# Optimization experiments

Measured on AMD Instinct MI355X. Metric: run time of the kernel, lower is better.

## Reference

```python
import jax, jax.numpy as jnp
import numpy as np

NUM_HEADS = 16

def setup_inputs() -> dict:
    key = jax.random.key(0)
    k1, k2, k3 = jax.random.split(key, 3)
    D = 1024
    return {
        "hidden_states": jax.random.normal(k1, (2, 2048, D), dtype=jnp.float32),
        "c_attn_w": jax.random.normal(k2, (D, 3 * D), dtype=jnp.float32) * 0.02,
        "c_attn_b": jnp.zeros((3 * D,), dtype=jnp.float32),
        "c_proj_w": jax.random.normal(k3, (D, D), dtype=jnp.float32) * 0.02,
        "c_proj_b": jnp.zeros((D,), dtype=jnp.float32),
    }

def reference(hidden_states, c_attn_w, c_attn_b, c_proj_w, c_proj_b):
    B, S, D = hidden_states.shape
    H = NUM_HEADS
    hd = D // H
    # Conv1D: x @ W + b, then split into q, k, v
    qkv = hidden_states @ c_attn_w + c_attn_b  # [B, S, 3D]
    q, k, v = jnp.split(qkv, 3, axis=-1)
    q = q.reshape(B, S, H, hd).transpose(0, 2, 1, 3)  # [B, H, S, hd]
    k = k.reshape(B, S, H, hd).transpose(0, 2, 1, 3)
    v = v.reshape(B, S, H, hd).transpose(0, 2, 1, 3)
    # scaled QK^T
    scores = jnp.einsum("bhqd,bhkd->bhqk", q, k) / jnp.asarray(hd ** 0.5, q.dtype)
    # causal mask (tril), masked positions set to dtype min per original code
    causal = jnp.tril(jnp.ones((S, S), dtype=bool))
    mask_value = jnp.finfo(scores.dtype).min
    scores = jnp.where(causal[None, None], scores, mask_value)
    attn = jax.nn.softmax(scores, axis=-1)
    out = jnp.einsum("bhqk,bhkd->bhqd", attn, v)  # [B, H, S, hd]
    out = out.transpose(0, 2, 1, 3).reshape(B, S, D)
    out = out @ c_proj_w + c_proj_b
    return out
```

## Files before the change

### kernel.cpp

```cpp
#include <hip/hip_runtime.h>
#include <hip/hip_bf16.h>
#include <math.h>

#define B_ 2
#define S_ 2048
#define D_ 1024
#define H_ 16
#define HD 64
#define M_ (B_ * S_)
#define N_QKV (3 * D_)

typedef short short8 __attribute__((ext_vector_type(8)));
typedef float floatx4 __attribute__((ext_vector_type(4)));

static __device__ __forceinline__ unsigned short f2bf(float x) {
    __hip_bfloat16 h = __float2bfloat16(x);
    unsigned short u;
    __builtin_memcpy(&u, &h, sizeof(u));
    return u;
}
static __device__ __forceinline__ float bf2f(unsigned short b) {
    union { unsigned u; float f; } v; v.u = ((unsigned)b) << 16;
    return v.f;
}
static __device__ __forceinline__ void split2(float x, unsigned short& h, unsigned short& l) {
    h = f2bf(x);
    l = f2bf(x - bf2f(h));
}

static __device__ __forceinline__ void dma16(const void* g, void* l) {
    __builtin_amdgcn_global_load_lds(
        (const __attribute__((address_space(1))) unsigned int*)g,
        (__attribute__((address_space(3))) unsigned int*)l,
        16, 0, 0);
}

__global__ __launch_bounds__(256) void prep_wT(
    const float* __restrict__ W, int N,
    unsigned short* __restrict__ Thi, unsigned short* __restrict__ Tlo)
{
    __shared__ float Ws[64][68];
    const int t  = threadIdx.x;
    const int n0 = blockIdx.x * 64, k0 = blockIdx.y * 64;
    {
        const int kl = t >> 4, nl = (t & 15) * 4;
        const float* src = W + (size_t)(k0 + kl) * N + n0 + nl;
#pragma unroll
        for (int g = 0; g < 4; g++)
            *(float4*)&Ws[kl + g * 16][nl] = *(const float4*)(src + (size_t)g * 16 * N);
    }
    __syncthreads();
    {
        const int nl = t >> 2, ks = (t & 3) * 16;
        short8 h0, h1, l0, l1;
#pragma unroll
        for (int j = 0; j < 8; j++) {
            unsigned short hh, ll;
            split2(Ws[ks + j][nl], hh, ll);
            h0[j] = (short)hh; l0[j] = (short)ll;
        }
#pragma unroll
        for (int j = 0; j < 8; j++) {
            unsigned short hh, ll;
            split2(Ws[ks + 8 + j][nl], hh, ll);
            h1[j] = (short)hh; l1[j] = (short)ll;
        }
        unsigned short* dh = Thi + (size_t)(n0 + nl) * D_ + k0 + ks;
        unsigned short* dl = Tlo + (size_t)(n0 + nl) * D_ + k0 + ks;
        *(short8*)dh = h0; *(short8*)(dh + 8) = h1;
        *(short8*)dl = l0; *(short8*)(dl + 8) = l1;
    }
}

__global__ __launch_bounds__(256) void gemm_qkv(
    const float* __restrict__ A,
    const unsigned short* __restrict__ BThi, const unsigned short* __restrict__ BTlo,
    const float* __restrict__ bias,
    unsigned short* __restrict__ Qhi, unsigned short* __restrict__ Qlo,
    unsigned short* __restrict__ Khi, unsigned short* __restrict__ Klo,
    unsigned short* __restrict__ vThi, unsigned short* __restrict__ vTlo)
{
    __shared__ unsigned short sAh[2][128 * 32], sAl[2][128 * 32];
    __shared__ unsigned short sBh[2][128 * 32], sBl[2][128 * 32];

    const int t    = threadIdx.x;
    const int m0   = blockIdx.y * 128, n0 = blockIdx.x * 128;
    const int lane = t & 63, wave = t >> 6;
    const int lm   = lane & 15, quad = lane >> 4;
    const int wm   = (wave >> 1) * 64, wn = (wave & 1) * 64;

    const int srow = t >> 1, sseg = (t & 1) * 16;
    const float* Ap = A + (size_t)(m0 + srow) * D_ + sseg;

    const int lrow = lane >> 2, lcol = (lane & 3) * 8;
    const unsigned short* gBh0 = BThi + (size_t)(n0 + wave * 32 + lrow) * D_ + lcol;
    const unsigned short* gBl0 = BTlo + (size_t)(n0 + wave * 32 + lrow) * D_ + lcol;
    const int ldst = wave * 1024 + lane * 8;

    floatx4 acc[4][4];
#pragma unroll
    for (int i = 0; i < 4; i++)
#pragma unroll
        for (int j = 0; j < 4; j++)
#pragma unroll
            for (int r = 0; r < 4; r++) acc[i][j][r] = 0.f;

    float4 af[4];
    af[0] = *(const float4*)(Ap);     af[1] = *(const float4*)(Ap + 4);
    af[2] = *(const float4*)(Ap + 8); af[3] = *(const float4*)(Ap + 12);

#define CVT_WRITE_A(BUF)                                                        \
    {                                                                           \
        short8 ah0, ah1, al0, al1;                                              \
        float xs0[8] = {af[0].x, af[0].y, af[0].z, af[0].w,                     \
                        af[1].x, af[1].y, af[1].z, af[1].w};                    \
        float xs1[8] = {af[2].x, af[2].y, af[2].z, af[2].w,                     \
                        af[3].x, af[3].y, af[3].z, af[3].w};                    \
        _Pragma("unroll")                                                       \
        for (int e = 0; e < 8; e++) {                                           \
            unsigned short hh, ll;                                              \
            split2(xs0[e], hh, ll); ah0[e] = (short)hh; al0[e] = (short)ll;     \
            split2(xs1[e], hh, ll); ah1[e] = (short)hh; al1[e] = (short)ll;     \
        }                                                                       \
        unsigned short* a_ = &sAh[BUF][srow * 32 + sseg];                       \
        unsigned short* b_ = &sAl[BUF][srow * 32 + sseg];                       \
        *(short8*)a_ = ah0; *(short8*)(a_ + 8) = ah1;                           \
        *(short8*)b_ = al0; *(short8*)(b_ + 8) = al1;                           \
    }

#define DMA_B(BUF, K0)                                                          \
    {                                                                           \
        dma16(gBh0 + (K0), &sBh[BUF][ldst]);                                    \
        dma16(gBh0 + (size_t)16 * D_ + (K0), &sBh[BUF][ldst + 512]);            \
        dma16(gBl0 + (K0), &sBl[BUF][ldst]);                                    \
        dma16(gBl0 + (size_t)16 * D_ + (K0), &sBl[BUF][ldst + 512]);            \
    }

    CVT_WRITE_A(0);
    DMA_B(0, 0);
    {
        const float* an = Ap + 32;
        af[0] = *(const float4*)(an);     af[1] = *(const float4*)(an + 4);
        af[2] = *(const float4*)(an + 8); af[3] = *(const float4*)(an + 12);
    }
    __syncthreads();

    int cur = 0;
    for (int k0 = 0; k0 < D_; k0 += 32) {
        if (k0 + 32 < D_) {
            DMA_B(cur ^ 1, k0 + 32);
            CVT_WRITE_A(cur ^ 1);
            if (k0 + 64 < D_) {
                const float* an = Ap + k0 + 64;
                af[0] = *(const float4*)(an);     af[1] = *(const float4*)(an + 4);
                af[2] = *(const float4*)(an + 8); af[3] = *(const float4*)(an + 12);
            }
        }

        short8 bhf[4], blf[4];
#pragma unroll
        for (int nb = 0; nb < 4; nb++) {
            const int r = wn + nb * 16 + lm;
            bhf[nb] = *(const short8*)&sBh[cur][r * 32 + quad * 8];
            blf[nb] = *(const short8*)&sBl[cur][r * 32 + quad * 8];
        }
#pragma unroll
        for (int mb = 0; mb < 4; mb++) {
            const int r = wm + mb * 16 + lm;
            short8 ah = *(const short8*)&sAh[cur][r * 32 + quad * 8];
            short8 al = *(const short8*)&sAl[cur][r * 32 + quad * 8];
#pragma unroll
            for (int nb = 0; nb < 4; nb++) {
                acc[mb][nb] = __builtin_amdgcn_mfma_f32_16x16x32_bf16(ah, bhf[nb], acc[mb][nb], 0, 0, 0);
                acc[mb][nb] = __builtin_amdgcn_mfma_f32_16x16x32_bf16(al, bhf[nb], acc[mb][nb], 0, 0, 0);
                acc[mb][nb] = __builtin_amdgcn_mfma_f32_16x16x32_bf16(ah, blf[nb], acc[mb][nb], 0, 0, 0);
            }
        }
        __syncthreads();
        cur ^= 1;
    }
#undef CVT_WRITE_A
#undef DMA_B

    const int nmode = n0 >> 10;
    if (nmode == 0) {
#pragma unroll
        for (int nb = 0; nb < 4; nb++) {
            const int c = n0 + wn + nb * 16 + lm;
            const float bv = bias[c];
#pragma unroll
            for (int mb = 0; mb < 4; mb++) {
                const int rowb = m0 + wm + mb * 16 + quad * 4;
#pragma unroll
                for (int r = 0; r < 4; r++) {
                    unsigned short hh, ll;
                    split2((acc[mb][nb][r] + bv) * 0.125f, hh, ll);
                    Qhi[(size_t)(rowb + r) * D_ + c] = hh;
                    Qlo[(size_t)(rowb + r) * D_ + c] = ll;
                }
            }
        }
    } else if (nmode == 1) {
#pragma unroll
        for (int nb = 0; nb < 4; nb++) {
            const int c = n0 + wn + nb * 16 + lm;
            const float bv = bias[c];
            const int cq = c - 1024;
#pragma unroll
            for (int mb = 0; mb < 4; mb++) {
                const int rowb = m0 + wm + mb * 16 + quad * 4;
#pragma unroll
                for (int r = 0; r < 4; r++) {
                    unsigned short hh, ll;
                    split2(acc[mb][nb][r] + bv, hh, ll);
                    Khi[(size_t)(rowb + r) * D_ + cq] = hh;
                    Klo[(size_t)(rowb + r) * D_ + cq] = ll;
                }
            }
        }
    } else {
#pragma unroll
        for (int nb = 0; nb < 4; nb++) {
            const int c = n0 + wn + nb * 16 + lm;
            const float bv = bias[c];
            const int cq = c - 2048;
            const int hh_ = cq >> 6, dd = cq & 63;
#pragma unroll
            for (int mb = 0; mb < 4; mb++) {
                const int rowb = m0 + wm + mb * 16 + quad * 4;
                const int bb = rowb >> 11, ss = rowb & 2047;
                unsigned short hv[4], lv[4];
#pragma unroll
                for (int r = 0; r < 4; r++)
                    split2(acc[mb][nb][r] + bv, hv[r], lv[r]);
                const size_t idx = ((size_t)((bb * 16 + hh_) * 64 + dd)) * S_ + ss;
                *(uint2*)&vThi[idx] = make_uint2((unsigned)hv[0] | ((unsigned)hv[1] << 16),
                                                 (unsigned)hv[2] | ((unsigned)hv[3] << 16));
                *(uint2*)&vTlo[idx] = make_uint2((unsigned)lv[0] | ((unsigned)lv[1] << 16),
                                                 (unsigned)lv[2] | ((unsigned)lv[3] << 16));
            }
        }
    }
}

__global__ __launch_bounds__(256) void gemm_out(
    const unsigned short* __restrict__ Ahi, const unsigned short* __restrict__ Alo,
    const unsigned short* __restrict__ BThi, const unsigned short* __restrict__ BTlo,
    const float* __restrict__ bias, float* __restrict__ C)
{
    __shared__ unsigned short sAh[2][128 * 32], sAl[2][128 * 32];
    __shared__ unsigned short sBh[2][64 * 32],  sBl[2][64 * 32];

    const int t   = threadIdx.x;
    const int lid = blockIdx.x;
    const int swz = (lid & 7) * 64 + (lid >> 3);
    const int bx  = swz & 15, by = swz >> 4;
    const int m0  = by * 128, n0 = bx * 64;
    const int lane = t & 63, wave = t >> 6;
    const int lm   = lane & 15, quad = lane >> 4;
    const int wm   = (wave >> 1) * 64, wn = (wave & 1) * 32;

    const int lrow = lane >> 2, lcol = (lane & 3) * 8;
    const unsigned short* gAh = Ahi + (size_t)(m0 + wave * 32 + lrow) * D_ + lcol;
    const unsigned short* gAl = Alo + (size_t)(m0 + wave * 32 + lrow) * D_ + lcol;
    const unsigned short* gBh = BThi + (size_t)(n0 + (t >> 2)) * D_ + (t & 3) * 8;
    const unsigned short* gBl = BTlo + (size_t)(n0 + (t >> 2)) * D_ + (t & 3) * 8;
    const int adst = wave * 1024 + lane * 8;
    const int bdst = t * 8;

#define STAGE_OUT(BUF, K0)                                                      \
    {                                                                           \
        dma16(gAh + (K0), &sAh[BUF][adst]);                                     \
        dma16(gAh + (size_t)16 * D_ + (K0), &sAh[BUF][adst + 512]);             \
        dma16(gAl + (K0), &sAl[BUF][adst]);                                     \
        dma16(gAl + (size_t)16 * D_ + (K0), &sAl[BUF][adst + 512]);             \
        dma16(gBh + (K0), &sBh[BUF][bdst]);                                     \
        dma16(gBl + (K0), &sBl[BUF][bdst]);                                     \
    }

    floatx4 acc[4][2];
#pragma unroll
    for (int i = 0; i < 4; i++)
#pragma unroll
        for (int j = 0; j < 2; j++)
#pragma unroll
            for (int r = 0; r < 4; r++) acc[i][j][r] = 0.f;

    STAGE_OUT(0, 0);
    __syncthreads();

    int cur = 0;
    for (int k0 = 0; k0 < D_; k0 += 32) {
        if (k0 + 32 < D_) STAGE_OUT(cur ^ 1, k0 + 32);

        short8 bhf[2], blf[2];
#pragma unroll
        for (int nb = 0; nb < 2; nb++) {
            const int r = wn + nb * 16 + lm;
            bhf[nb] = *(const short8*)&sBh[cur][r * 32 + quad * 8];
            blf[nb] = *(const short8*)&sBl[cur][r * 32 + quad * 8];
        }
#pragma unroll
        for (int mb = 0; mb < 4; mb++) {
            const int r = wm + mb * 16 + lm;
            short8 ah = *(const short8*)&sAh[cur][r * 32 + quad * 8];
            short8 al = *(const short8*)&sAl[cur][r * 32 + quad * 8];
#pragma unroll
            for (int nb = 0; nb < 2; nb++) {
                acc[mb][nb] = __builtin_amdgcn_mfma_f32_16x16x32_bf16(ah, bhf[nb], acc[mb][nb], 0, 0, 0);
                acc[mb][nb] = __builtin_amdgcn_mfma_f32_16x16x32_bf16(al, bhf[nb], acc[mb][nb], 0, 0, 0);
                acc[mb][nb] = __builtin_amdgcn_mfma_f32_16x16x32_bf16(ah, blf[nb], acc[mb][nb], 0, 0, 0);
            }
        }
        __syncthreads();
        cur ^= 1;
    }
#undef STAGE_OUT

#pragma unroll
    for (int nb = 0; nb < 2; nb++) {
        const int col = n0 + wn + nb * 16 + lm;
        const float bv = bias[col];
#pragma unroll
        for (int mb = 0; mb < 4; mb++) {
            const int rowb = m0 + wm + mb * 16 + quad * 4;
#pragma unroll
            for (int r = 0; r < 4; r++)
                C[(size_t)(rowb + r) * D_ + col] = acc[mb][nb][r] + bv;
        }
    }
}

#define PST 72

__global__ __launch_bounds__(512, 2) void flash_attn_mfma(
    unsigned short* QAhi, unsigned short* QAlo,
    const unsigned short* __restrict__ Khi, const unsigned short* __restrict__ Klo,
    const unsigned short* __restrict__ vThi, const unsigned short* __restrict__ vTlo)
{
    __shared__ unsigned short KhS[2][64 * PST];
    __shared__ unsigned short KlS[2][64 * PST];
    __shared__ unsigned short VhS[2][64 * PST];
    __shared__ unsigned short VlS[2][64 * PST];
    __shared__ unsigned short PhS[128 * PST];
    __shared__ unsigned short PlS[128 * PST];

    const int t    = threadIdx.x;
    const int pj   = blockIdx.x;
    const int bh   = blockIdx.y;
    const int b    = bh >> 4, h = bh & 15;
    const int lane = t & 63, w = t >> 6;
    const int lm   = lane & 15, quad = lane >> 4;

    const int srow = t >> 3;
    const int sseg = (t & 7) * 8;

    const unsigned short* Kh_b = Khi + (size_t)(b * S_) * D_ + h * HD + sseg;
    const unsigned short* Kl_b = Klo + (size_t)(b * S_) * D_ + h * HD + sseg;
    const unsigned short* Vh_b = vThi + ((size_t)((b * 16 + h) * 64 + srow)) * S_ + sseg;
    const unsigned short* Vl_b = vTlo + ((size_t)((b * 16 + h) * 64 + srow)) * S_ + sseg;

    const int sdst = srow * PST + sseg;

    for (int phse = 0; phse < 2; phse++) {
        const int qt = phse ? (15 - pj) : pj;
        const int q0 = qt * 128;
        const int ntiles = 2 * qt + 2;
        const int wdiag = (q0 >> 6) + (w >> 2);

        short8 qh[2], ql[2];
        {
            const size_t qoff = (size_t)(b * S_ + q0 + 16 * w + lm) * D_ + h * HD + quad * 8;
            qh[0] = *(const short8*)&QAhi[qoff];
            qh[1] = *(const short8*)&QAhi[qoff + 32];
            ql[0] = *(const short8*)&QAlo[qoff];
            ql[1] = *(const short8*)&QAlo[qoff + 32];
        }

        float lsum[4] = {0.f, 0.f, 0.f, 0.f};
        floatx4 o[4];
#pragma unroll
        for (int nb = 0; nb < 4; nb++)
#pragma unroll
            for (int r = 0; r < 4; r++) o[nb][r] = 0.f;

        uint4 pkh, pkl, pvh, pvl;
        pkh = *(const uint4*)(Kh_b + (size_t)srow * D_);
        pkl = *(const uint4*)(Kl_b + (size_t)srow * D_);
        pvh = *(const uint4*)(Vh_b);
        pvl = *(const uint4*)(Vl_b);
        *(uint4*)&KhS[0][sdst] = pkh;
        *(uint4*)&KlS[0][sdst] = pkl;
        *(uint4*)&VhS[0][sdst] = pvh;
        *(uint4*)&VlS[0][sdst] = pvl;
        if (ntiles > 1) {
            pkh = *(const uint4*)(Kh_b + (size_t)(64 + srow) * D_);
            pkl = *(const uint4*)(Kl_b + (size_t)(64 + srow) * D_);
            pvh = *(const uint4*)(Vh_b + 64);
            pvl = *(const uint4*)(Vl_b + 64);
        }
        __syncthreads();

        int cur = 0;
        for (int kt = 0; kt < ntiles; kt++) {
            if (kt + 1 < ntiles) {
                *(uint4*)&KhS[cur ^ 1][sdst] = pkh;
                *(uint4*)&KlS[cur ^ 1][sdst] = pkl;
                *(uint4*)&VhS[cur ^ 1][sdst] = pvh;
                *(uint4*)&VlS[cur ^ 1][sdst] = pvl;
            }
            if (kt + 2 < ntiles) {
                const int k1 = (kt + 2) * 64;
                pkh = *(const uint4*)(Kh_b + (size_t)(k1 + srow) * D_);
                pkl = *(const uint4*)(Kl_b + (size_t)(k1 + srow) * D_);
                pvh = *(const uint4*)(Vh_b + k1);
                pvl = *(const uint4*)(Vl_b + k1);
            }

            if (kt <= wdiag) {
                floatx4 sa[4];
#pragma unroll
                for (int nb = 0; nb < 4; nb++)
#pragma unroll
                    for (int r = 0; r < 4; r++) sa[nb][r] = 0.f;
                __builtin_amdgcn_s_setprio(1);
#pragma unroll
                for (int s = 0; s < 2; s++) {
#pragma unroll
                    for (int nb = 0; nb < 4; nb++) {
                        short8 kh = *(const short8*)&KhS[cur][(nb * 16 + lm) * PST + s * 32 + quad * 8];
                        short8 kl = *(const short8*)&KlS[cur][(nb * 16 + lm) * PST + s * 32 + quad * 8];
                        sa[nb] = __builtin_amdgcn_mfma_f32_16x16x32_bf16(qh[s], kh, sa[nb], 0, 0, 0);
                        sa[nb] = __builtin_amdgcn_mfma_f32_16x16x32_bf16(ql[s], kh, sa[nb], 0, 0, 0);
                        sa[nb] = __builtin_amdgcn_mfma_f32_16x16x32_bf16(qh[s], kl, sa[nb], 0, 0, 0);
                    }
                }
                __builtin_amdgcn_s_setprio(0);

                const bool diag = (kt == wdiag);
                const int kbase = kt * 64;
#pragma unroll
                for (int r = 0; r < 4; r++) {
                    const int qabs = q0 + 16 * w + 4 * quad + r;
                    const int rloc = 16 * w + 4 * quad + r;
#pragma unroll
                    for (int nb = 0; nb < 4; nb++) {
                        float p = __expf(sa[nb][r]);
                        if (diag && (kbase + 16 * nb + lm > qabs)) p = 0.f;
                        lsum[r] += p;
                        unsigned short hh, ll;
                        split2(p, hh, ll);
                        PhS[rloc * PST + 16 * nb + lm] = hh;
                        PlS[rloc * PST + 16 * nb + lm] = ll;
                    }
                }

                __builtin_amdgcn_s_setprio(1);
#pragma unroll
                for (int ks = 0; ks < 2; ks++) {
                    short8 pf = *(const short8*)&PhS[(16 * w + lm) * PST + ks * 32 + quad * 8];
                    short8 pg = *(const short8*)&PlS[(16 * w + lm) * PST + ks * 32 + quad * 8];
#pragma unroll
                    for (int nb = 0; nb < 4; nb++) {
                        short8 vhf = *(const short8*)&VhS[cur][(16 * nb + lm) * PST + ks * 32 + quad * 8];
                        short8 vlf = *(const short8*)&VlS[cur][(16 * nb + lm) * PST + ks * 32 + quad * 8];
                        o[nb] = __builtin_amdgcn_mfma_f32_16x16x32_bf16(pf, vhf, o[nb], 0, 0, 0);
                        o[nb] = __builtin_amdgcn_mfma_f32_16x16x32_bf16(pg, vhf, o[nb], 0, 0, 0);
                        o[nb] = __builtin_amdgcn_mfma_f32_16x16x32_bf16(pf, vlf, o[nb], 0, 0, 0);
                    }
                }
                __builtin_amdgcn_s_setprio(0);
            }
            __syncthreads();
            cur ^= 1;
        }

#pragma unroll
        for (int r = 0; r < 4; r++) {
            float l = lsum[r];
            l += __shfl_xor(l, 1);
            l += __shfl_xor(l, 2);
            l += __shfl_xor(l, 4);
            l += __shfl_xor(l, 8);
            const float inv = 1.f / l;
            const size_t rowoff =
                (size_t)(b * S_ + q0 + 16 * w + 4 * quad + r) * D_ + h * HD + lm;
#pragma unroll
            for (int nb = 0; nb < 4; nb++) {
                unsigned short hh, ll;
                split2(o[nb][r] * inv, hh, ll);
                QAhi[rowoff + 16 * nb] = hh;
                QAlo[rowoff + 16 * nb] = ll;
            }
        }
    }
}

extern "C" void kernel_launch(void* const* d_in, const int* in_sizes, int n_in,
                              void* d_out, int out_size, void* d_ws, size_t ws_size,
                              hipStream_t stream)
{
    const float* hs     = (const float*)d_in[0];
    const float* attn_w = (const float*)d_in[1];
    const float* attn_b = (const float*)d_in[2];
    const float* proj_w = (const float*)d_in[3];
    const float* proj_b = (const float*)d_in[4];
    float* outp = (float*)d_out;

    const size_t QE = (size_t)M_ * D_;
    const size_t WQ = (size_t)D_ * N_QKV;
    unsigned short* Qhi   = (unsigned short*)d_ws;
    unsigned short* Qlo   = Qhi + QE;
    unsigned short* Khi   = Qlo + QE;
    unsigned short* Klo   = Khi + QE;
    unsigned short* vThi  = Klo + QE;
    unsigned short* vTlo  = vThi + QE;
    unsigned short* WqThi = vTlo + QE;
    unsigned short* WqTlo = WqThi + WQ;
    unsigned short* WpThi = WqTlo + WQ;
    unsigned short* WpTlo = WpThi + (size_t)D_ * D_;

    dim3 blk(256);
    prep_wT<<<dim3(N_QKV / 64, D_ / 64), blk, 0, stream>>>(attn_w, N_QKV, WqThi, WqTlo);
    prep_wT<<<dim3(D_ / 64, D_ / 64), blk, 0, stream>>>(proj_w, D_, WpThi, WpTlo);
    gemm_qkv<<<dim3(N_QKV / 128, M_ / 128), blk, 0, stream>>>(
        hs, WqThi, WqTlo, attn_b, Qhi, Qlo, Khi, Klo, vThi, vTlo);
    flash_attn_mfma<<<dim3(8, B_ * H_), dim3(512), 0, stream>>>(
        Qhi, Qlo, Khi, Klo, vThi, vTlo);
    gemm_out<<<dim3(512), blk, 0, stream>>>(
        Qhi, Qlo, WpThi, WpTlo, proj_b, outp);
}
```

Baseline: 319.9 us.

## Pre-split activations to bf16 hi/lo and single-buffer GEMM LDS staging

Adds a prep_A kernel that splits the fp32 hidden states into bf16 hi/lo arrays once, so gemm_qkv loads A through direct global-to-LDS DMA instead of converting in-register on every tile. Both GEMMs drop their double-buffered LDS pipeline for a single buffer with a sync before and after each DMA stage. This halves LDS use, which may raise occupancy, and removes redundant per-tile conversion work. The cost is an extra kernel with an additional read and write of the activations, plus load latency that is no longer overlapped with MFMA compute.

After: 316.1 us. No clear change (-1.2%).

```diff
diff --git a/kernel.cpp b/kernel.cpp
--- a/kernel.cpp
+++ b/kernel.cpp
@@ -35,6 +35,25 @@
         16, 0, 0);
 }
 
+__global__ __launch_bounds__(256) void prep_A(
+    const float* __restrict__ X,
+    unsigned short* __restrict__ Ahi, unsigned short* __restrict__ Alo)
+{
+    const size_t i = ((size_t)blockIdx.x * 256 + threadIdx.x) * 8;
+    float4 a = *(const float4*)(X + i);
+    float4 b = *(const float4*)(X + i + 4);
+    float xs[8] = {a.x, a.y, a.z, a.w, b.x, b.y, b.z, b.w};
+    short8 h, l;
+#pragma unroll
+    for (int e = 0; e < 8; e++) {
+        unsigned short hh, ll;
+        split2(xs[e], hh, ll);
+        h[e] = (short)hh; l[e] = (short)ll;
+    }
+    *(short8*)&Ahi[i] = h;
+    *(short8*)&Alo[i] = l;
+}
+
 __global__ __launch_bounds__(256) void prep_wT(
     const float* __restrict__ W, int N,
     unsigned short* __restrict__ Thi, unsigned short* __restrict__ Tlo)
@@ -73,15 +92,15 @@
 }
 
 __global__ __launch_bounds__(256) void gemm_qkv(
-    const float* __restrict__ A,
+    const unsigned short* __restrict__ Ahi, const unsigned short* __restrict__ Alo,
     const unsigned short* __restrict__ BThi, const unsigned short* __restrict__ BTlo,
     const float* __restrict__ bias,
     unsigned short* __restrict__ Qhi, unsigned short* __restrict__ Qlo,
     unsigned short* __restrict__ Khi, unsigned short* __restrict__ Klo,
     unsigned short* __restrict__ vThi, unsigned short* __restrict__ vTlo)
 {
-    __shared__ unsigned short sAh[2][128 * 32], sAl[2][128 * 32];
-    __shared__ unsigned short sBh[2][128 * 32], sBl[2][128 * 32];
+    __shared__ unsigned short sAh[128 * 32], sAl[128 * 32];
+    __shared__ unsigned short sBh[128 * 32], sBl[128 * 32];
 
     const int t    = threadIdx.x;
     const int m0   = blockIdx.y * 128, n0 = blockIdx.x * 128;
@@ -89,12 +108,11 @@
     const int lm   = lane & 15, quad = lane >> 4;
     const int wm   = (wave >> 1) * 64, wn = (wave & 1) * 64;
 
-    const int srow = t >> 1, sseg = (t & 1) * 16;
-    const float* Ap = A + (size_t)(m0 + srow) * D_ + sseg;
-
     const int lrow = lane >> 2, lcol = (lane & 3) * 8;
-    const unsigned short* gBh0 = BThi + (size_t)(n0 + wave * 32 + lrow) * D_ + lcol;
-    const unsigned short* gBl0 = BTlo + (size_t)(n0 + wave * 32 + lrow) * D_ + lcol;
+    const unsigned short* gAh = Ahi + (size_t)(m0 + wave * 32 + lrow) * D_ + lcol;
+    const unsigned short* gAl = Alo + (size_t)(m0 + wave * 32 + lrow) * D_ + lcol;
+    const unsigned short* gBh = BThi + (size_t)(n0 + wave * 32 + lrow) * D_ + lcol;
+    const unsigned short* gBl = BTlo + (size_t)(n0 + wave * 32 + lrow) * D_ + lcol;
     const int ldst = wave * 1024 + lane * 8;
 
     floatx4 acc[4][4];
@@ -105,70 +123,30 @@
 #pragma unroll
             for (int r = 0; r < 4; r++) acc[i][j][r] = 0.f;
 
-    float4 af[4];
-    af[0] = *(const float4*)(Ap);     af[1] = *(const float4*)(Ap + 4);
-    af[2] = *(const float4*)(Ap + 8); af[3] = *(const float4*)(Ap + 12);
-
-#define CVT_WRITE_A(BUF)                                                        \
-    {                                                                           \
-        short8 ah0, ah1, al0, al1;                                              \
-        float xs0[8] = {af[0].x, af[0].y, af[0].z, af[0].w,                     \
-                        af[1].x, af[1].y, af[1].z, af[1].w};                    \
-        float xs1[8] = {af[2].x, af[2].y, af[2].z, af[2].w,                     \
-                        af[3].x, af[3].y, af[3].z, af[3].w};                    \
-        _Pragma("unroll")                                                       \
-        for (int e = 0; e < 8; e++) {                                           \
-            unsigned short hh, ll;                                              \
-            split2(xs0[e], hh, ll); ah0[e] = (short)hh; al0[e] = (short)ll;     \
-            split2(xs1[e], hh, ll); ah1[e] = (short)hh; al1[e] = (short)ll;     \
-        }                                                                       \
-        unsigned short* a_ = &sAh[BUF][srow * 32 + sseg];                       \
-        unsigned short* b_ = &sAl[BUF][srow * 32 + sseg];                       \
-        *(short8*)a_ = ah0; *(short8*)(a_ + 8) = ah1;                           \
-        *(short8*)b_ = al0; *(short8*)(b_ + 8) = al1;                           \
-    }
-
-#define DMA_B(BUF, K0)                                                          \
-    {                                                                           \
-        dma16(gBh0 + (K0), &sBh[BUF][ldst]);                                    \
-        dma16(gBh0 + (size_t)16 * D_ + (K0), &sBh[BUF][ldst + 512]);            \
-        dma16(gBl0 + (K0), &sBl[BUF][ldst]);                                    \
-        dma16(gBl0 + (size_t)16 * D_ + (K0), &sBl[BUF][ldst + 512]);            \
-    }
-
-    CVT_WRITE_A(0);
-    DMA_B(0, 0);
-    {
-        const float* an = Ap + 32;
-        af[0] = *(const float4*)(an);     af[1] = *(const float4*)(an + 4);
-        af[2] = *(const float4*)(an + 8); af[3] = *(const float4*)(an + 12);
-    }
-    __syncthreads();
-
-    int cur = 0;
     for (int k0 = 0; k0 < D_; k0 += 32) {
-        if (k0 + 32 < D_) {
-            DMA_B(cur ^ 1, k0 + 32);
-            CVT_WRITE_A(cur ^ 1);
-            if (k0 + 64 < D_) {
-                const float* an = Ap + k0 + 64;
-                af[0] = *(const float4*)(an);     af[1] = *(const float4*)(an + 4);
-                af[2] = *(const float4*)(an + 8); af[3] = *(const float4*)(an + 12);
-            }
-        }
+        __syncthreads();
+        dma16(gAh + k0, &sAh[ldst]);
+        dma16(gAh + (size_t)16 * D_ + k0, &sAh[ldst + 512]);
+        dma16(gAl + k0, &sAl[ldst]);
+        dma16(gAl + (size_t)16 * D_ + k0, &sAl[ldst + 512]);
+        dma16(gBh + k0, &sBh[ldst]);
+        dma16(gBh + (size_t)16 * D_ + k0, &sBh[ldst + 512]);
+        dma16(gBl + k0, &sBl[ldst]);
+        dma16(gBl + (size_t)16 * D_ + k0, &sBl[ldst + 512]);
+        __syncthreads();
 
         short8 bhf[4], blf[4];
 #pragma unroll
         for (int nb = 0; nb < 4; nb++) {
             const int r = wn + nb * 16 + lm;
-            bhf[nb] = *(const short8*)&sBh[cur][r * 32 + quad * 8];
-            blf[nb] = *(const short8*)&sBl[cur][r * 32 + quad * 8];
+            bhf[nb] = *(const short8*)&sBh[r * 32 + quad * 8];
+            blf[nb] = *(const short8*)&sBl[r * 32 + quad * 8];
         }
 #pragma unroll
         for (int mb = 0; mb < 4; mb++) {
             const int r = wm + mb * 16 + lm;
-            short8 ah = *(const short8*)&sAh[cur][r * 32 + quad * 8];
-            short8 al = *(const short8*)&sAl[cur][r * 32 + quad * 8];
+            short8 ah = *(const short8*)&sAh[r * 32 + quad * 8];
+            short8 al = *(const short8*)&sAl[r * 32 + quad * 8];
 #pragma unroll
             for (int nb = 0; nb < 4; nb++) {
                 acc[mb][nb] = __builtin_amdgcn_mfma_f32_16x16x32_bf16(ah, bhf[nb], acc[mb][nb], 0, 0, 0);
@@ -176,11 +154,7 @@
                 acc[mb][nb] = __builtin_amdgcn_mfma_f32_16x16x32_bf16(ah, blf[nb], acc[mb][nb], 0, 0, 0);
             }
         }
-        __syncthreads();
-        cur ^= 1;
-    }
-#undef CVT_WRITE_A
-#undef DMA_B
+    }
 
     const int nmode = n0 >> 10;
     if (nmode == 0) {
@@ -248,8 +222,8 @@
     const unsigned short* __restrict__ BThi, const unsigned short* __restrict__ BTlo,
     const float* __restrict__ bias, float* __restrict__ C)
 {
-    __shared__ unsigned short sAh[2][128 * 32], sAl[2][128 * 32];
-    __shared__ unsigned short sBh[2][64 * 32],  sBl[2][64 * 32];
+    __shared__ unsigned short sAh[128 * 32], sAl[128 * 32];
+    __shared__ unsigned short sBh[64 * 32],  sBl[64 * 32];
 
     const int t   = threadIdx.x;
     const int lid = blockIdx.x;
@@ -268,16 +242,6 @@
     const int adst = wave * 1024 + lane * 8;
     const int bdst = t * 8;
 
-#define STAGE_OUT(BUF, K0)                                                      \
-    {                                                                           \
-        dma16(gAh + (K0), &sAh[BUF][adst]);                                     \
-        dma16(gAh + (size_t)16 * D_ + (K0), &sAh[BUF][adst + 512]);             \
-        dma16(gAl + (K0), &sAl[BUF][adst]);                                     \
-        dma16(gAl + (size_t)16 * D_ + (K0), &sAl[BUF][adst + 512]);             \
-        dma16(gBh + (K0), &sBh[BUF][bdst]);                                     \
-        dma16(gBl + (K0), &sBl[BUF][bdst]);                                     \
-    }
-
     floatx4 acc[4][2];
 #pragma unroll
     for (int i = 0; i < 4; i++)
@@ -286,25 +250,28 @@
 #pragma unroll
             for (int r = 0; r < 4; r++) acc[i][j][r] = 0.f;
 
-    STAGE_OUT(0, 0);
-    __syncthreads();
-
-    int cur = 0;
     for (int k0 = 0; k0 < D_; k0 += 32) {
-        if (k0 + 32 < D_) STAGE_OUT(cur ^ 1, k0 + 32);
+        __syncthreads();
+        dma16(gAh + k0, &sAh[adst]);
+        dma16(gAh + (size_t)16 * D_ + k0, &sAh[adst + 512]);
+        dma16(gAl + k0, &sAl[adst]);
+        dma16(gAl + (size_t)16 * D_ + k0, &sAl[adst + 512]);
+        dma16(gBh + k0, &sBh[bdst]);
+        dma16(gBl + k0, &sBl[bdst]);
+        __syncthreads();
 
         short8 bhf[2], blf[2];
 #pragma unroll
         for (int nb = 0; nb < 2; nb++) {
             const int r = wn + nb * 16 + lm;
-            bhf[nb] = *(const short8*)&sBh[cur][r * 32 + quad * 8];
-            blf[nb] = *(const short8*)&sBl[cur][r * 32 + quad * 8];
+            bhf[nb] = *(const short8*)&sBh[r * 32 + quad * 8];
+            blf[nb] = *(const short8*)&sBl[r * 32 + quad * 8];
         }
 #pragma unroll
         for (int mb = 0; mb < 4; mb++) {
             const int r = wm + mb * 16 + lm;
-            short8 ah = *(const short8*)&sAh[cur][r * 32 + quad * 8];
-            short8 al = *(const short8*)&sAl[cur][r * 32 + quad * 8];
+            short8 ah = *(const short8*)&sAh[r * 32 + quad * 8];
+            short8 al = *(const short8*)&sAl[r * 32 + quad * 8];
 #pragma unroll
             for (int nb = 0; nb < 2; nb++) {
                 acc[mb][nb] = __builtin_amdgcn_mfma_f32_16x16x32_bf16(ah, bhf[nb], acc[mb][nb], 0, 0, 0);
@@ -312,10 +279,7 @@
                 acc[mb][nb] = __builtin_amdgcn_mfma_f32_16x16x32_bf16(ah, blf[nb], acc[mb][nb], 0, 0, 0);
             }
         }
-        __syncthreads();
-        cur ^= 1;
-    }
-#undef STAGE_OUT
+    }
 
 #pragma unroll
     for (int nb = 0; nb < 2; nb++) {
@@ -519,12 +483,15 @@
     unsigned short* WqTlo = WqThi + WQ;
     unsigned short* WpThi = WqTlo + WQ;
     unsigned short* WpTlo = WpThi + (size_t)D_ * D_;
+    unsigned short* Ahi   = WpTlo + (size_t)D_ * D_;
+    unsigned short* Alo   = Ahi + QE;
 
     dim3 blk(256);
+    prep_A<<<dim3(M_ * D_ / 2048), blk, 0, stream>>>(hs, Ahi, Alo);
     prep_wT<<<dim3(N_QKV / 64, D_ / 64), blk, 0, stream>>>(attn_w, N_QKV, WqThi, WqTlo);
     prep_wT<<<dim3(D_ / 64, D_ / 64), blk, 0, stream>>>(proj_w, D_, WpThi, WpTlo);
     gemm_qkv<<<dim3(N_QKV / 128, M_ / 128), blk, 0, stream>>>(
-        hs, WqThi, WqTlo, attn_b, Qhi, Qlo, Khi, Klo, vThi, vTlo);
+        Ahi, Alo, WqThi, WqTlo, attn_b, Qhi, Qlo, Khi, Klo, vThi, vTlo);
     flash_attn_mfma<<<dim3(8, B_ * H_), dim3(512), 0, stream>>>(
         Qhi, Qlo, Khi, Klo, vThi, vTlo);
     gemm_out<<<dim3(512), blk, 0, stream>>>(
```
